# Kernel optimization log

Measured on AMD Instinct MI355X. Metric: run time of the kernel, lower is better.

Reference implementation:

```python
import jax, jax.numpy as jnp
import numpy as np

RES = 32
EPS = 0.0


def setup_inputs() -> dict:
    key = jax.random.key(0)
    k1, k2 = jax.random.split(key)
    B, C, N = 32, 64, 8192
    features = jax.random.normal(k1, (B, C, N), dtype=jnp.float32)
    coords = jax.random.normal(k2, (B, 3, N), dtype=jnp.float32)
    return {"features": features, "coords": coords}


def reference(features, coords):
    R = RES
    B, C, N = features.shape
    # center coords per batch (mean over points)
    norm_coords = coords - jnp.mean(coords, axis=2, keepdims=True)  # [B,3,N]
    # normalize=True branch: divide by 2*max point L2 norm
    max_norm = jnp.max(jnp.linalg.norm(norm_coords, axis=1, keepdims=True),
                       axis=2, keepdims=True)  # [B,1,1]
    norm_coords = norm_coords / (max_norm * 2.0 + EPS) + 0.5
    # scale to voxel grid and clip
    norm_coords = jnp.clip(norm_coords * R, 0.0, R - 1)  # [B,3,N]
    vox = jnp.round(norm_coords).astype(jnp.int32)  # [B,3,N]
    # flat voxel index per point, offset per batch -> global segment id
    flat = (vox[:, 0] * R + vox[:, 1]) * R + vox[:, 2]  # [B,N]
    idx = (flat + jnp.arange(B, dtype=jnp.int32)[:, None] * (R ** 3)).reshape(-1)  # [B*N]
    num_seg = B * R ** 3
    cnt = jax.ops.segment_sum(jnp.ones((B * N,), features.dtype), idx,
                              num_segments=num_seg)  # [B*R^3]
    feat_pn = features.transpose(0, 2, 1).reshape(B * N, C)  # [B*N,C]
    sums = jax.ops.segment_sum(feat_pn, idx, num_segments=num_seg)  # [B*R^3,C]
    avg = sums / jnp.maximum(cnt, 1.0)[:, None]
    voxelized = avg.reshape(B, R, R, R, C).transpose(0, 4, 1, 2, 3)  # [B,C,R,R,R]
    return voxelized, norm_coords
```

## Files before the change

### kernel.cpp

```cpp
#include <hip/hip_runtime.h>

constexpr int B = 32, C = 64, N = 8192, R = 32, R3 = R * R * R;
constexpr int HALF = R3 / 2;
constexpr int T = 1024;
constexpr int PPT = N / T;

constexpr size_t CNT_OFF = 0;
constexpr size_t IDX_OFF = (size_t)B * R3 * 4;
constexpr size_t PF_OFF  = IDX_OFF + (size_t)B * N * 2;
constexpr size_t PRM_OFF = PF_OFF + (size_t)B * N * 4;

__global__ __launch_bounds__(1024) void stats_kernel(
    const float* __restrict__ coords, float* __restrict__ params) {
  const int b = blockIdx.x;
  const int t = threadIdx.x;
  const float* cb = coords + (size_t)b * 3 * N;
  __shared__ double sm[1024];
  __shared__ float smf[1024];

  double sx = 0.0, sy = 0.0, sz = 0.0;
  for (int n = t; n < N; n += 1024) {
    sx += (double)cb[n];
    sy += (double)cb[N + n];
    sz += (double)cb[2 * N + n];
  }
  float mean[3];
  double vals[3] = {sx, sy, sz};
  for (int d = 0; d < 3; ++d) {
    sm[t] = vals[d];
    __syncthreads();
    for (int s = 512; s > 0; s >>= 1) {
      if (t < s) sm[t] += sm[t + s];
      __syncthreads();
    }
    mean[d] = (float)(sm[0] / (double)N);
    __syncthreads();
  }

  float mx = 0.0f;
  for (int n = t; n < N; n += 1024) {
    float dx = __fsub_rn(cb[n], mean[0]);
    float dy = __fsub_rn(cb[N + n], mean[1]);
    float dz = __fsub_rn(cb[2 * N + n], mean[2]);
    float n2 = __fadd_rn(__fadd_rn(__fmul_rn(dx, dx), __fmul_rn(dy, dy)),
                         __fmul_rn(dz, dz));
    mx = fmaxf(mx, n2);
  }
  smf[t] = mx;
  __syncthreads();
  for (int s = 512; s > 0; s >>= 1) {
    if (t < s) smf[t] = fmaxf(smf[t], smf[t + s]);
    __syncthreads();
  }
  if (t == 0) {
    float maxn = __fsqrt_rn(smf[0]);
    params[b * 4 + 0] = mean[0];
    params[b * 4 + 1] = mean[1];
    params[b * 4 + 2] = mean[2];
    params[b * 4 + 3] = __fmul_rn(maxn, 2.0f);
  }
}

__global__ __launch_bounds__(256) void voxelize_kernel(
    const float* __restrict__ coords, const float* __restrict__ params,
    float* __restrict__ ncout, unsigned short* __restrict__ idx,
    unsigned int* __restrict__ cnt) {
  const int i = blockIdx.x * 256 + threadIdx.x;
  const int b = i >> 13;
  const int n = i & (N - 1);
  const float* cb = coords + (size_t)b * 3 * N;
  const float m0 = params[b * 4 + 0];
  const float m1 = params[b * 4 + 1];
  const float m2 = params[b * 4 + 2];
  const float dn = params[b * 4 + 3];

  float t0 = __fmul_rn(__fadd_rn(__fdiv_rn(__fsub_rn(cb[n], m0), dn), 0.5f), 32.0f);
  float t1 = __fmul_rn(__fadd_rn(__fdiv_rn(__fsub_rn(cb[N + n], m1), dn), 0.5f), 32.0f);
  float t2 = __fmul_rn(__fadd_rn(__fdiv_rn(__fsub_rn(cb[2 * N + n], m2), dn), 0.5f), 32.0f);
  t0 = fminf(fmaxf(t0, 0.0f), 31.0f);
  t1 = fminf(fmaxf(t1, 0.0f), 31.0f);
  t2 = fminf(fmaxf(t2, 0.0f), 31.0f);

  ncout[(size_t)b * 3 * N + n] = t0;
  ncout[(size_t)b * 3 * N + N + n] = t1;
  ncout[(size_t)b * 3 * N + 2 * N + n] = t2;

  const int vx = (int)rintf(t0);
  const int vy = (int)rintf(t1);
  const int vz = (int)rintf(t2);
  const int flat = (vx * R + vy) * R + vz;
  idx[i] = (unsigned short)flat;
  atomicAdd(&cnt[b * R3 + flat], 1u);
}

__global__ __launch_bounds__(256) void invp_kernel(
    const unsigned short* __restrict__ idx,
    const unsigned int* __restrict__ cnt, float* __restrict__ pf) {
  const int i = blockIdx.x * 256 + threadIdx.x;
  const int b = i >> 13;
  const unsigned int k = cnt[b * R3 + (int)idx[i]];
  pf[i] = __fdiv_rn(1.0f, (float)(k ? k : 1u));
}

__global__ __launch_bounds__(1024, 8) void accum_kernel(
    const float* __restrict__ feats, const unsigned short* __restrict__ idx,
    const float* __restrict__ pf, float* __restrict__ voxout) {
  __shared__ float lds[HALF];
  const int blk = blockIdx.x;
  const int c = blk & (C - 1);
  const int b = blk >> 6;
  const int t = threadIdx.x;

  const unsigned short* ib = idx + (size_t)b * N;
  const float* pb = pf + (size_t)b * N;
  const float* fb = feats + ((size_t)b * C + c) * N;
  int iv[PPT];
  float fv[PPT];
#pragma unroll
  for (int k = 0; k < PPT; ++k) {
    const int n = t + k * T;
    iv[k] = (int)ib[n];
    fv[k] = fb[n] * pb[n];
  }

  float4* lp = (float4*)lds;
  const float4 z = {0.f, 0.f, 0.f, 0.f};

  for (int h = 0; h < 2; ++h) {
    const int lo = h * HALF;

#pragma unroll
    for (int k = t; k < HALF / 4; k += T) lp[k] = z;
    __syncthreads();

#pragma unroll
    for (int k = 0; k < PPT; ++k) {
      const int loc = iv[k] - lo;
      if ((unsigned)loc < (unsigned)HALF) atomicAdd(&lds[loc], fv[k]);
    }
    __syncthreads();

    float4* ob4 = (float4*)(voxout + ((size_t)b * C + c) * R3 + lo);
#pragma unroll
    for (int v = t; v < HALF / 4; v += T) ob4[v] = lp[v];
    __syncthreads();
  }
}

extern "C" void kernel_launch(void* const* d_in, const int* in_sizes, int n_in,
                              void* d_out, int out_size, void* d_ws,
                              size_t ws_size, hipStream_t stream) {
  const float* feats  = (const float*)d_in[0];
  const float* coords = (const float*)d_in[1];

  float* voxout = (float*)d_out;
  float* ncout  = voxout + (size_t)B * C * R3;

  char* ws = (char*)d_ws;
  unsigned int* cnt   = (unsigned int*)(ws + CNT_OFF);
  unsigned short* idx = (unsigned short*)(ws + IDX_OFF);
  float* pf           = (float*)(ws + PF_OFF);
  float* params       = (float*)(ws + PRM_OFF);

  hipMemsetAsync(cnt, 0, (size_t)B * R3 * sizeof(unsigned int), stream);
  stats_kernel<<<B, 1024, 0, stream>>>(coords, params);
  voxelize_kernel<<<(B * N) / 256, 256, 0, stream>>>(coords, params, ncout,
                                                     idx, cnt);
  invp_kernel<<<(B * N) / 256, 256, 0, stream>>>(idx, cnt, pf);
  accum_kernel<<<B * C, 1024, 0, stream>>>(feats, idx, pf, voxout);
}
```

Baseline: 378.6 us.

## Split accum LDS into quarters with 512 threads and vectorized loads

The accumulation kernel now uses a 32KB LDS buffer covering a quarter of the voxel grid and makes four passes with 512-thread blocks instead of two passes over a 64KB half with 1024 threads. Index, feature and scale loads are widened to 32-bit and float2 pairs, and the LDS is cleared during the write-out pass so one sync is saved per pass. The smaller LDS footprint is meant to let more blocks run per CU, at the cost of more passes over the per-thread point registers and more bounds checks.

```diff
diff --git a/kernel.cpp b/kernel.cpp
--- a/kernel.cpp
+++ b/kernel.cpp
@@ -1,8 +1,8 @@
 #include <hip/hip_runtime.h>
 
 constexpr int B = 32, C = 64, N = 8192, R = 32, R3 = R * R * R;
-constexpr int HALF = R3 / 2;
-constexpr int T = 1024;
+constexpr int QUAR = R3 / 4;
+constexpr int T = 512;
 constexpr int PPT = N / T;
 
 constexpr size_t CNT_OFF = 0;
@@ -102,47 +102,55 @@
   pf[i] = __fdiv_rn(1.0f, (float)(k ? k : 1u));
 }
 
-__global__ __launch_bounds__(1024, 8) void accum_kernel(
+__global__ __launch_bounds__(512, 8) void accum_kernel(
     const float* __restrict__ feats, const unsigned short* __restrict__ idx,
     const float* __restrict__ pf, float* __restrict__ voxout) {
-  __shared__ float lds[HALF];
+  __shared__ float lds[QUAR];
   const int blk = blockIdx.x;
   const int c = blk & (C - 1);
   const int b = blk >> 6;
   const int t = threadIdx.x;
 
-  const unsigned short* ib = idx + (size_t)b * N;
-  const float* pb = pf + (size_t)b * N;
-  const float* fb = feats + ((size_t)b * C + c) * N;
-  int iv[PPT];
-  float fv[PPT];
+  const unsigned int* ib32 = (const unsigned int*)(idx + (size_t)b * N);
+  const float2* pb2 = (const float2*)(pf + (size_t)b * N);
+  const float2* fb2 = (const float2*)(feats + ((size_t)b * C + c) * N);
+  unsigned int ivw[PPT / 2];
+  float2 fv2[PPT / 2];
 #pragma unroll
-  for (int k = 0; k < PPT; ++k) {
-    const int n = t + k * T;
-    iv[k] = (int)ib[n];
-    fv[k] = fb[n] * pb[n];
+  for (int k = 0; k < PPT / 2; ++k) {
+    const int j = t + k * T;
+    ivw[k] = ib32[j];
+    const float2 f = fb2[j];
+    const float2 p = pb2[j];
+    fv2[k] = {f.x * p.x, f.y * p.y};
   }
 
   float4* lp = (float4*)lds;
   const float4 z = {0.f, 0.f, 0.f, 0.f};
 
-  for (int h = 0; h < 2; ++h) {
-    const int lo = h * HALF;
+#pragma unroll
+  for (int k = t; k < QUAR / 4; k += T) lp[k] = z;
+  __syncthreads();
+
+  for (int h = 0; h < 4; ++h) {
+    const int lo = h * QUAR;
 
 #pragma unroll
-    for (int k = t; k < HALF / 4; k += T) lp[k] = z;
-    __syncthreads();
-
-#pragma unroll
-    for (int k = 0; k < PPT; ++k) {
-      const int loc = iv[k] - lo;
-      if ((unsigned)loc < (unsigned)HALF) atomicAdd(&lds[loc], fv[k]);
+    for (int k = 0; k < PPT / 2; ++k) {
+      const int i0 = (int)(ivw[k] & 0xFFFFu) - lo;
+      const int i1 = (int)(ivw[k] >> 16) - lo;
+      if ((unsigned)i0 < (unsigned)QUAR) atomicAdd(&lds[i0], fv2[k].x);
+      if ((unsigned)i1 < (unsigned)QUAR) atomicAdd(&lds[i1], fv2[k].y);
     }
     __syncthreads();
 
     float4* ob4 = (float4*)(voxout + ((size_t)b * C + c) * R3 + lo);
 #pragma unroll
-    for (int v = t; v < HALF / 4; v += T) ob4[v] = lp[v];
+    for (int v = t; v < QUAR / 4; v += T) {
+      const float4 o = lp[v];
+      lp[v] = z;
+      ob4[v] = o;
+    }
     __syncthreads();
   }
 }
@@ -167,5 +175,5 @@
   voxelize_kernel<<<(B * N) / 256, 256, 0, stream>>>(coords, params, ncout,
                                                      idx, cnt);
   invp_kernel<<<(B * N) / 256, 256, 0, stream>>>(idx, cnt, pf);
-  accum_kernel<<<B * C, 1024, 0, stream>>>(feats, idx, pf, voxout);
+  accum_kernel<<<B * C, T, 0, stream>>>(feats, idx, pf, voxout);
 }
```

New measurement: 380.2 us. No clear change (+0.4%).
